# Performance work log

Measured on AMD Instinct MI355X. Metric: run time of the kernel, lower is better.

## Reference

```python
import jax, jax.numpy as jnp
import numpy as np

N, E, IN_DIM, HID, HEADS, LAYERS, NTYPES, NGRAPH = 50000, 600000, 64, 128, 8, 3, 10, 500
C = HID // HEADS
NEG_SLOPE = 0.2
EPS = 1e-5


def setup_inputs() -> dict:
    key = jax.random.key(0)
    ks = jax.random.split(key, 24)
    inp = {
        "x": jax.random.normal(ks[0], (N, IN_DIM), jnp.float32),
        "edge_index": jax.random.randint(ks[1], (2, E), 0, N),
        "node_types": jax.random.randint(ks[2], (N,), 0, NTYPES),
        "batch": jnp.sort(jax.random.randint(ks[3], (N,), 0, NGRAPH)),
        # node embedding linear
        "emb_W": jax.random.normal(ks[4], (IN_DIM, HID), jnp.float32) / np.sqrt(IN_DIM),
        "emb_b": jnp.zeros((HID,), jnp.float32),
        "ntype_emb": jax.random.normal(ks[5], (NTYPES, HID), jnp.float32) * 0.02,
        # stacked GAT layer params
        "gat_W": jax.random.normal(ks[6], (LAYERS, HID, HID), jnp.float32) / np.sqrt(HID),
        "att_src": jax.random.normal(ks[7], (LAYERS, HEADS, C), jnp.float32) * 0.1,
        "att_dst": jax.random.normal(ks[8], (LAYERS, HEADS, C), jnp.float32) * 0.1,
        "gat_b": jnp.zeros((LAYERS, HID), jnp.float32),
        "ln_g": jnp.ones((LAYERS, HID), jnp.float32),
        "ln_b": jnp.zeros((LAYERS, HID), jnp.float32),
        # global attention MLP
        "ga_W1": jax.random.normal(ks[9], (HID, HID), jnp.float32) / np.sqrt(HID),
        "ga_b1": jnp.zeros((HID,), jnp.float32),
        "ga_W2": jax.random.normal(ks[10], (HID, 1), jnp.float32) / np.sqrt(HID),
        "ga_b2": jnp.zeros((1,), jnp.float32),
        # graph classifier head
        "cls_W1": jax.random.normal(ks[11], (HID, HID), jnp.float32) / np.sqrt(HID),
        "cls_b1": jnp.zeros((HID,), jnp.float32),
        "cls_W2": jax.random.normal(ks[12], (HID, 1), jnp.float32) / np.sqrt(HID),
        "cls_b2": jnp.zeros((1,), jnp.float32),
    }
    return inp


def _layer_norm(h, g, b):
    mu = jnp.mean(h, axis=-1, keepdims=True)
    var = jnp.mean(jnp.square(h - mu), axis=-1, keepdims=True)
    return (h - mu) * jax.lax.rsqrt(var + EPS) * g + b


def _gat_layer(h, src, dst, W, a_src, a_dst, bias):
    # h: [N, HID] -> per-head projection [N, H, C]
    hp = (h @ W).reshape(N, HEADS, C)
    alpha_s = jnp.sum(hp * a_src, axis=-1)  # [N, H]
    alpha_d = jnp.sum(hp * a_dst, axis=-1)  # [N, H]
    e = jax.nn.leaky_relu(alpha_s[src] + alpha_d[dst], NEG_SLOPE)  # [E', H]
    # segment softmax over incoming edges of each destination node
    m = jax.ops.segment_max(e, dst, num_segments=N)
    ex = jnp.exp(e - m[dst])
    s = jax.ops.segment_sum(ex, dst, num_segments=N)
    alpha = ex / s[dst]  # every node has a self-loop, so s > 0
    msg = hp[src] * alpha[:, :, None]  # [E', H, C]
    out = jax.ops.segment_sum(msg, dst, num_segments=N)  # [N, H, C]
    return out.reshape(N, HID) + bias


def reference(x, edge_index, node_types, batch, emb_W, emb_b, ntype_emb,
              gat_W, att_src, att_dst, gat_b, ln_g, ln_b,
              ga_W1, ga_b1, ga_W2, ga_b2, cls_W1, cls_b1, cls_W2, cls_b2):
    # self-loops (PyG GATConv add_self_loops=True)
    loop = jnp.arange(N)
    src = jnp.concatenate([edge_index[0], loop])
    dst = jnp.concatenate([edge_index[1], loop])

    h = x @ emb_W + emb_b
    h = h + ntype_emb[node_types]

    for l in range(LAYERS):
        h_prev = h
        h = _gat_layer(h, src, dst, gat_W[l], att_src[l], att_dst[l], gat_b[l])
        h = _layer_norm(h, ln_g[l], ln_b[l])
        h = jax.nn.relu(h + h_prev)

    # global attention pooling: softmax over all nodes (dim 0, as in source)
    scores = jnp.tanh(h @ ga_W1 + ga_b1) @ ga_W2 + ga_b2  # [N, 1]
    attw = jax.nn.softmax(scores, axis=0)
    h_graph = jnp.sum(h * attw, axis=0)  # [HID]

    # global mean pool per graph
    sums = jax.ops.segment_sum(h, batch, num_segments=NGRAPH)  # [G, HID]
    cnts = jax.ops.segment_sum(jnp.ones((N, 1), h.dtype), batch, num_segments=NGRAPH)
    mean_pool = sums / jnp.maximum(cnts, 1.0)

    hg = h_graph + mean_pool  # broadcast [HID] + [G, HID]

    # graph classifier head (features_batch=None path), squeeze(-1)
    out = jax.nn.relu(hg @ cls_W1 + cls_b1) @ cls_W2 + cls_b2
    return out.squeeze(-1)  # [G]
```

## Files before the change

kernel.cpp:

```cpp
#include <hip/hip_runtime.h>
#include <hip/hip_bf16.h>
#include <math.h>

#define HID 128
#define HEADS 8
#define INDIM 64

typedef _Float16 f16x8 __attribute__((ext_vector_type(8)));
typedef _Float16 f16x4 __attribute__((ext_vector_type(4)));
typedef _Float16 f16x2 __attribute__((ext_vector_type(2)));
typedef float f32x4 __attribute__((ext_vector_type(4)));

__device__ __forceinline__ float fast_tanh(float x) {
    return 1.f - 2.f / (__expf(2.f * x) + 1.f);
}

#if defined(__has_builtin)
#if __has_builtin(__builtin_amdgcn_fdot2)
#define HAVE_FDOT2 1
#endif
#endif


__global__ void count_kernel(const int* __restrict__ ei, int* __restrict__ deg, int E, int EE) {
    int e = blockIdx.x * blockDim.x + threadIdx.x;
    if (e >= EE) return;
    int dst = (e < E) ? ei[E + e] : (e - E);
    atomicAdd(&deg[dst], 1);
}

__global__ void block_sum_kernel(const int* __restrict__ deg, int* __restrict__ partials, int N) {
    __shared__ int sdata[4];
    int t = threadIdx.x;
    int i = blockIdx.x * 256 + t;
    int v = (i < N) ? deg[i] : 0;
#pragma unroll
    for (int m = 32; m >= 1; m >>= 1) v += __shfl_xor(v, m, 64);
    if ((t & 63) == 0) sdata[t >> 6] = v;
    __syncthreads();
    if (t == 0) partials[blockIdx.x] = sdata[0] + sdata[1] + sdata[2] + sdata[3];
}

__global__ void scan_partials_kernel(int* __restrict__ partials, int nb) {
    int lane = threadIdx.x;
    int carry = 0;
    for (int base = 0; base < nb; base += 64) {
        int i = base + lane;
        int v = (i < nb) ? partials[i] : 0;
        int orig = v;
#pragma unroll
        for (int off = 1; off < 64; off <<= 1) {
            int x = __shfl_up(v, off, 64);
            if (lane >= off) v += x;
        }
        if (i < nb) partials[i] = v - orig + carry;
        carry += __shfl(v, 63, 64);
    }
}

__global__ void rowptr_kernel(const int* __restrict__ deg, const int* __restrict__ partials,
                              int* __restrict__ rowptr, int* __restrict__ woff, int N, int EE) {
    __shared__ int tmp[256];
    int t = threadIdx.x;
    int i = blockIdx.x * 256 + t;
    int v = (i < N) ? deg[i] : 0;
    tmp[t] = v;
    __syncthreads();
#pragma unroll
    for (int off = 1; off < 256; off <<= 1) {
        int x = (t >= off) ? tmp[t - off] : 0;
        __syncthreads();
        tmp[t] += x;
        __syncthreads();
    }
    int excl = tmp[t] - v + partials[blockIdx.x];
    if (i < N) { rowptr[i] = excl; woff[i] = excl; }
    if (blockIdx.x == 0 && t == 0) rowptr[N] = EE;
}

__global__ void scatter_kernel(const int* __restrict__ ei, int* __restrict__ woff,
                               int* __restrict__ esrc, int E, int EE) {
    int e = blockIdx.x * blockDim.x + threadIdx.x;
    if (e >= EE) return;
    int src, dst;
    if (e < E) { src = ei[e]; dst = ei[E + e]; } else { src = dst = e - E; }
    int slot = atomicAdd(&woff[dst], 1);
    esrc[slot] = src;
}

__global__ void gstart_kernel(const int* __restrict__ batch, int* __restrict__ gstart,
                              int N, int G) {
    int g = blockIdx.x * blockDim.x + threadIdx.x;
    if (g > G) return;
    int lo = 0, hi = N;
    while (lo < hi) {
        int mid = (lo + hi) >> 1;
        if (batch[mid] < g) lo = mid + 1; else hi = mid;
    }
    gstart[g] = lo;
}

__global__ void convert_x_kernel(const float* __restrict__ x, _Float16* __restrict__ x16, int tot4) {
    int i = blockIdx.x * blockDim.x + threadIdx.x;
    if (i >= tot4) return;
    float4 v = ((const float4*)x)[i];
    f16x4 o; o[0] = (_Float16)v.x; o[1] = (_Float16)v.y; o[2] = (_Float16)v.z; o[3] = (_Float16)v.w;
    *(f16x4*)&x16[4 * i] = o;
}

__global__ void convert_w_kernel(const float* __restrict__ emb_W, const float* __restrict__ gat_W,
                                 const float* __restrict__ ga_W1, _Float16* __restrict__ wt_emb,
                                 _Float16* __restrict__ wt_gat, _Float16* __restrict__ wt_ga1) {
    int i = blockIdx.x * blockDim.x + threadIdx.x;
    if (i < 8192) {
        int k = i >> 7, n = i & 127;
        wt_emb[n * 64 + k] = (_Float16)emb_W[i];
    } else if (i < 8192 + 49152) {
        int j = i - 8192;
        int l = j >> 14, r = j & 16383;
        int k = r >> 7, n = r & 127;
        wt_gat[l * 16384 + n * 128 + k] = (_Float16)gat_W[j];
    } else if (i < 73728) {
        int j = i - 57344;
        int k = j >> 7, n = j & 127;
        wt_ga1[n * 128 + k] = (_Float16)ga_W1[j];
    }
}

__global__ __launch_bounds__(256) void mfma_proj_kernel(
    int mode, int K, int N,
    const _Float16* __restrict__ A16, const _Float16* __restrict__ Wt,
    const float* __restrict__ bias, const float* __restrict__ nemb,
    const int* __restrict__ ntypes, _Float16* __restrict__ h16out,
    const float* __restrict__ asrc, const float* __restrict__ adst,
    _Float16* __restrict__ hp_out, float* __restrict__ als, float* __restrict__ ald,
    const float* __restrict__ w2, const float* __restrict__ b2,
    float* __restrict__ escore)
{
    __shared__ _Float16 w_lds[128 * 136];
    __shared__ _Float16 a_lds[64 * 136];
    int t = threadIdx.x;
    int n0 = blockIdx.x * 64;
    int KP = K + 8;

    int K8 = K >> 3;
    for (int i = t; i < 128 * K8; i += 256) {
        int row = i / K8, c8 = i - row * K8;
        *(f16x8*)&w_lds[row * KP + 8 * c8] = *(const f16x8*)&Wt[(size_t)row * K + 8 * c8];
    }
    for (int i = t; i < 64 * K8; i += 256) {
        int row = i / K8, c8 = i - row * K8;
        f16x8 v = {};
        if (n0 + row < N) v = *(const f16x8*)&A16[(size_t)(n0 + row) * K + 8 * c8];
        *(f16x8*)&a_lds[row * KP + 8 * c8] = v;
    }
    __syncthreads();

    int lane = t & 63, wv = t >> 6;
    int l15 = lane & 15, quad = lane >> 4;

    f32x4 acc[8];
#pragma unroll
    for (int c = 0; c < 8; ++c) acc[c] = (f32x4){0.f, 0.f, 0.f, 0.f};

    int ksteps = K >> 5;
    for (int kk = 0; kk < ksteps; ++kk) {
        f16x8 af = *(const f16x8*)&a_lds[(wv * 16 + l15) * KP + kk * 32 + quad * 8];
#pragma unroll
        for (int c = 0; c < 8; ++c) {
            f16x8 bf = *(const f16x8*)&w_lds[(c * 16 + l15) * KP + kk * 32 + quad * 8];
            acc[c] = __builtin_amdgcn_mfma_f32_16x16x32_f16(af, bf, acc[c], 0, 0, 0);
        }
    }

    if (mode == 0) {
        float bv[8];
#pragma unroll
        for (int c = 0; c < 8; ++c) bv[c] = bias[c * 16 + l15];
        __syncthreads();
#pragma unroll
        for (int r = 0; r < 4; ++r) {
            int n = n0 + wv * 16 + quad * 4 + r;
            int nt = (n < N) ? ntypes[n] : 0;
#pragma unroll
            for (int c = 0; c < 8; ++c)
                a_lds[(wv * 16 + quad * 4 + r) * 136 + c * 16 + l15] =
                    (_Float16)(acc[c][r] + bv[c] + nemb[nt * HID + c * 16 + l15]);
        }
        __syncthreads();
        for (int i = t; i < 64 * 16; i += 256) {
            int row = i >> 4, c8 = i & 15;
            int n = n0 + row;
            if (n < N) *(f16x8*)&h16out[(size_t)n * HID + 8 * c8] = *(const f16x8*)&a_lds[row * 136 + 8 * c8];
        }
    } else if (mode == 1) {
        __syncthreads();
#pragma unroll
        for (int c = 0; c < 8; ++c)
#pragma unroll
            for (int r = 0; r < 4; ++r)
                a_lds[(wv * 16 + quad * 4 + r) * 136 + c * 16 + l15] = (_Float16)acc[c][r];
        __syncthreads();
        for (int i = t; i < 64 * 16; i += 256) {
            int row = i >> 4, c8 = i & 15;
            int n = n0 + row;
            if (n < N) *(f16x8*)&hp_out[(size_t)n * HID + 8 * c8] = *(const f16x8*)&a_lds[row * 136 + 8 * c8];
        }
        for (int task = t; task < 512; task += 256) {
            int row = task >> 3, hd = task & 7;
            int n = n0 + row;
            if (n >= N) continue;
            f16x8 v0 = *(const f16x8*)&a_lds[row * 136 + hd * 16];
            f16x8 v1 = *(const f16x8*)&a_lds[row * 136 + hd * 16 + 8];
            float va = 0.f, vd = 0.f;
#pragma unroll
            for (int j = 0; j < 8; ++j) {
                va += (float)v0[j] * asrc[hd * 16 + j] + (float)v1[j] * asrc[hd * 16 + 8 + j];
                vd += (float)v0[j] * adst[hd * 16 + j] + (float)v1[j] * adst[hd * 16 + 8 + j];
            }
            als[n * HEADS + hd] = va;
            ald[n * HEADS + hd] = vd;
        }
    } else {
        float b2v = b2[0];
        float treg[4] = {0.f, 0.f, 0.f, 0.f};
#pragma unroll
        for (int c = 0; c < 8; ++c) {
            float b1v = bias[c * 16 + l15];
            float w2v = w2[c * 16 + l15];
#pragma unroll
            for (int r = 0; r < 4; ++r)
                treg[r] += fast_tanh(acc[c][r] + b1v) * w2v;
        }
#pragma unroll
        for (int r = 0; r < 4; ++r) {
            float v = treg[r];
#pragma unroll
            for (int m = 8; m >= 1; m >>= 1) v += __shfl_xor(v, m, 64);
            if (l15 == 0) {
                int n = n0 + wv * 16 + quad * 4 + r;
                if (n < N) escore[n] = __expf(v + b2v);
            }
        }
    }
}

__global__ void gat_aggregate_kernel(const int* __restrict__ rowptr, const int* __restrict__ esrc,
                                     const float* __restrict__ als, const float* __restrict__ ald,
                                     const _Float16* __restrict__ hp16, const float* __restrict__ gb,
                                     const float* __restrict__ lg, const float* __restrict__ lb,
                                     _Float16* __restrict__ h16, int N) {
    int wave = threadIdx.x >> 6;
    int lane = threadIdx.x & 63;
    int n = blockIdx.x * 4 + wave;
    if (n >= N) return;
    int esub = lane >> 4;
    int cg = lane & 15;
    int hd = cg >> 1;
    float adv = ald[n * HEADS + hd];
    int row = rowptr[n], end = rowptr[n + 1];
    int last = end - 1;
    float acc[8] = {0.f, 0.f, 0.f, 0.f, 0.f, 0.f, 0.f, 0.f};
    float sw = 0.f;
    for (int base = row; base < end; base += 16) {
        int iA = base + esub;
        int iB = iA + 4, iC = iA + 8, iD = iA + 12;
        int cA = iA <= last ? iA : last;
        int cB = iB <= last ? iB : last;
        int cC = iC <= last ? iC : last;
        int cD = iD <= last ? iD : last;
        int sA = esrc[cA], sB = esrc[cB], sC = esrc[cC], sD = esrc[cD];
        f16x8 pA = *(const f16x8*)&hp16[(size_t)sA * HID + cg * 8];
        f16x8 pB = *(const f16x8*)&hp16[(size_t)sB * HID + cg * 8];
        f16x8 pC = *(const f16x8*)&hp16[(size_t)sC * HID + cg * 8];
        f16x8 pD = *(const f16x8*)&hp16[(size_t)sD * HID + cg * 8];
        float aA = als[sA * HEADS + hd];
        float aB = als[sB * HEADS + hd];
        float aC = als[sC * HEADS + hd];
        float aD = als[sD * HEADS + hd];
        float lA = aA + adv; lA = lA > 0.f ? lA : 0.2f * lA;
        float lB = aB + adv; lB = lB > 0.f ? lB : 0.2f * lB;
        float lC = aC + adv; lC = lC > 0.f ? lC : 0.2f * lC;
        float lD = aD + adv; lD = lD > 0.f ? lD : 0.2f * lD;
        float wA = __expf(lA) * ((iA < end) ? 1.f : 0.f);
        float wB = __expf(lB) * ((iB < end) ? 1.f : 0.f);
        float wC = __expf(lC) * ((iC < end) ? 1.f : 0.f);
        float wD = __expf(lD) * ((iD < end) ? 1.f : 0.f);
        sw += (wA + wB) + (wC + wD);
#ifdef HAVE_FDOT2
        f16x2 wAB; wAB[0] = (_Float16)wA; wAB[1] = (_Float16)wB;
        f16x2 wCD; wCD[0] = (_Float16)wC; wCD[1] = (_Float16)wD;
#pragma unroll
        for (int j = 0; j < 8; ++j) {
            f16x2 prAB; prAB[0] = pA[j]; prAB[1] = pB[j];
            f16x2 prCD; prCD[0] = pC[j]; prCD[1] = pD[j];
            acc[j] = __builtin_amdgcn_fdot2(prAB, wAB, acc[j], false);
            acc[j] = __builtin_amdgcn_fdot2(prCD, wCD, acc[j], false);
        }
#else
#pragma unroll
        for (int j = 0; j < 8; ++j)
            acc[j] += wA * (float)pA[j] + wB * (float)pB[j]
                    + wC * (float)pC[j] + wD * (float)pD[j];
#endif
    }
#pragma unroll
    for (int m = 16; m <= 32; m <<= 1) {
        sw += __shfl_xor(sw, m, 64);
#pragma unroll
        for (int j = 0; j < 8; ++j) acc[j] += __shfl_xor(acc[j], m, 64);
    }
    float inv_sw = 1.f / sw;
    float4 g0 = ((const float4*)(gb + cg * 8))[0];
    float4 g1 = ((const float4*)(gb + cg * 8))[1];
    float v[8];
    v[0] = acc[0] * inv_sw + g0.x; v[1] = acc[1] * inv_sw + g0.y;
    v[2] = acc[2] * inv_sw + g0.z; v[3] = acc[3] * inv_sw + g0.w;
    v[4] = acc[4] * inv_sw + g1.x; v[5] = acc[5] * inv_sw + g1.y;
    v[6] = acc[6] * inv_sw + g1.z; v[7] = acc[7] * inv_sw + g1.w;
    float s = 0.f;
#pragma unroll
    for (int j = 0; j < 8; ++j) s += v[j];
#pragma unroll
    for (int m = 32; m >= 1; m >>= 1) s += __shfl_xor(s, m, 64);
    float mu = s * (1.f / 512.f);
    float d[8], sq = 0.f;
#pragma unroll
    for (int j = 0; j < 8; ++j) { d[j] = v[j] - mu; sq += d[j] * d[j]; }
#pragma unroll
    for (int m = 32; m >= 1; m >>= 1) sq += __shfl_xor(sq, m, 64);
    float inv = rsqrtf(sq * (1.f / 512.f) + 1e-5f);
    float4 lg0 = ((const float4*)(lg + cg * 8))[0];
    float4 lg1 = ((const float4*)(lg + cg * 8))[1];
    float4 lb0 = ((const float4*)(lb + cg * 8))[0];
    float4 lb1 = ((const float4*)(lb + cg * 8))[1];
    float lgv[8] = {lg0.x, lg0.y, lg0.z, lg0.w, lg1.x, lg1.y, lg1.z, lg1.w};
    float lbv[8] = {lb0.x, lb0.y, lb0.z, lb0.w, lb1.x, lb1.y, lb1.z, lb1.w};
    f16x8 hold = *(const f16x8*)&h16[(size_t)n * HID + cg * 8];
    f16x8 hnew;
#pragma unroll
    for (int j = 0; j < 8; ++j) {
        float r = d[j] * inv * lgv[j] + lbv[j] + (float)hold[j];
        hnew[j] = (_Float16)(r > 0.f ? r : 0.f);
    }
    if (esub == 0) *(f16x8*)&h16[(size_t)n * HID + cg * 8] = hnew;
}

__global__ void pool_graph_kernel(const _Float16* __restrict__ h16, const float* __restrict__ escore,
                                  const int* __restrict__ gstart, float* __restrict__ sums,
                                  float* __restrict__ cnts, float* __restrict__ hgZ, int G) {
    int g = blockIdx.x;
    int t = threadIdx.x;
    int c = t & 127, grp = t >> 7;
    int s = gstart[g], e = gstart[g + 1];
    float msum = 0.f, asum = 0.f, z = 0.f;
    for (int n = s + grp; n < e; n += 4) {
        float hv = (float)h16[(size_t)n * HID + c];
        float es = escore[n];
        msum += hv;
        asum += es * hv;
        if (c == 0) z += es;
    }
    __shared__ float sm[4][HID];
    __shared__ float sa[4][HID];
    __shared__ float sz[4];
    sm[grp][c] = msum;
    sa[grp][c] = asum;
    if (c == 0) sz[grp] = z;
    __syncthreads();
    if (t < HID) {
        float m = sm[0][t] + sm[1][t] + sm[2][t] + sm[3][t];
        float a = sa[0][t] + sa[1][t] + sa[2][t] + sa[3][t];
        sums[(size_t)g * HID + t] = m;
        atomicAdd(&hgZ[t], a);
    } else if (t == HID) {
        cnts[g] = (float)(e - s);
        atomicAdd(&hgZ[HID], sz[0] + sz[1] + sz[2] + sz[3]);
    }
}

__global__ void head_kernel(const float* __restrict__ hgZ, const float* __restrict__ sums,
                            const float* __restrict__ cnts, const float* __restrict__ W1,
                            const float* __restrict__ b1, const float* __restrict__ W2,
                            const float* __restrict__ b2, float* __restrict__ out, int G) {
    int g = blockIdx.x;
    int t = threadIdx.x;
    __shared__ float hr[HID];
    __shared__ float part[2];
    float Z = hgZ[HID];
    float cnt = cnts[g];
    cnt = cnt > 1.f ? cnt : 1.f;
    hr[t] = hgZ[t] / Z + sums[(size_t)g * HID + t] / cnt;
    __syncthreads();
    float acc = b1[t];
#pragma unroll 8
    for (int k = 0; k < HID; ++k) acc += hr[k] * W1[k * HID + t];
    acc = acc > 0.f ? acc : 0.f;
    float v = acc * W2[t];
#pragma unroll
    for (int m = 32; m >= 1; m >>= 1) v += __shfl_xor(v, m, 64);
    if ((t & 63) == 0) part[t >> 6] = v;
    __syncthreads();
    if (t == 0) out[g] = part[0] + part[1] + b2[0];
}

extern "C" void kernel_launch(void* const* d_in, const int* in_sizes, int n_in,
                              void* d_out, int out_size, void* d_ws, size_t ws_size,
                              hipStream_t stream) {
    const float* x        = (const float*)d_in[0];
    const int*   ei       = (const int*)d_in[1];
    const int*   ntypes   = (const int*)d_in[2];
    const int*   batch    = (const int*)d_in[3];
    const float* emb_W    = (const float*)d_in[4];
    const float* emb_b    = (const float*)d_in[5];
    const float* nemb     = (const float*)d_in[6];
    const float* gat_W    = (const float*)d_in[7];
    const float* att_src  = (const float*)d_in[8];
    const float* att_dst  = (const float*)d_in[9];
    const float* gat_b    = (const float*)d_in[10];
    const float* ln_g     = (const float*)d_in[11];
    const float* ln_b     = (const float*)d_in[12];
    const float* ga_W1    = (const float*)d_in[13];
    const float* ga_b1    = (const float*)d_in[14];
    const float* ga_W2    = (const float*)d_in[15];
    const float* ga_b2    = (const float*)d_in[16];
    const float* cls_W1   = (const float*)d_in[17];
    const float* cls_b1   = (const float*)d_in[18];
    const float* cls_W2   = (const float*)d_in[19];
    const float* cls_b2   = (const float*)d_in[20];
    float* out = (float*)d_out;

    const int N  = in_sizes[2];
    const int E  = in_sizes[1] / 2;
    const int EE = E + N;
    const int G  = out_size;
    const int NB = (N + 255) / 256;

    float* ws      = (float*)d_ws;
    float* als     = ws;
    float* ald     = als + (size_t)N * HEADS;
    float* escore  = ald + (size_t)N * HEADS;
    float* sums    = escore + N;
    float* cnts    = sums + (size_t)G * HID;
    float* hgZ     = cnts + G;
    _Float16* h16  = (_Float16*)(hgZ + HID + 1);
    _Float16* hp16 = h16 + (size_t)N * HID;
    _Float16* x16  = hp16 + (size_t)N * HID;
    _Float16* wt_emb = x16 + (size_t)N * INDIM;
    _Float16* wt_gat = wt_emb + 128 * 64;
    _Float16* wt_ga1 = wt_gat + 3 * 128 * 128;
    int*   rowptr  = (int*)(wt_ga1 + 128 * 128);
    int*   woff    = rowptr + (N + 1);
    int*   deg     = woff + N;
    int*   esrc    = deg + N;
    int*   partials= esrc + EE;
    int*   gstart  = partials + NB;

    hipMemsetAsync(deg, 0, (size_t)N * sizeof(int), stream);
    hipMemsetAsync(hgZ, 0, (HID + 1) * sizeof(float), stream);
    count_kernel<<<(EE + 255) / 256, 256, 0, stream>>>(ei, deg, E, EE);
    block_sum_kernel<<<NB, 256, 0, stream>>>(deg, partials, N);
    scan_partials_kernel<<<1, 64, 0, stream>>>(partials, NB);
    rowptr_kernel<<<NB, 256, 0, stream>>>(deg, partials, rowptr, woff, N, EE);
    scatter_kernel<<<(EE + 255) / 256, 256, 0, stream>>>(ei, woff, esrc, E, EE);
    gstart_kernel<<<(G + 64) / 64, 64, 0, stream>>>(batch, gstart, N, G);
    convert_x_kernel<<<(N * INDIM / 4 + 255) / 256, 256, 0, stream>>>(x, x16, N * INDIM / 4);
    convert_w_kernel<<<(73728 + 255) / 256, 256, 0, stream>>>(
        emb_W, gat_W, ga_W1, wt_emb, wt_gat, wt_ga1);

    const int PB = (N + 63) / 64;

    mfma_proj_kernel<<<PB, 256, 0, stream>>>(
        0, INDIM, N, x16, wt_emb, emb_b, nemb, ntypes, h16,
        nullptr, nullptr, nullptr, nullptr, nullptr, nullptr, nullptr, nullptr);

    for (int l = 0; l < 3; ++l) {
        mfma_proj_kernel<<<PB, 256, 0, stream>>>(
            1, HID, N, h16, wt_gat + (size_t)l * HID * HID,
            nullptr, nullptr, nullptr, nullptr,
            att_src + l * HID, att_dst + l * HID,
            hp16, als, ald, nullptr, nullptr, nullptr);
        gat_aggregate_kernel<<<(N + 3) / 4, 256, 0, stream>>>(
            rowptr, esrc, als, ald, hp16,
            gat_b + l * HID, ln_g + l * HID, ln_b + l * HID, h16, N);
    }

    mfma_proj_kernel<<<PB, 256, 0, stream>>>(
        2, HID, N, h16, wt_ga1, ga_b1, nullptr, nullptr, nullptr,
        nullptr, nullptr, nullptr, nullptr, nullptr, ga_W2, ga_b2, escore);

    pool_graph_kernel<<<G, 512, 0, stream>>>(h16, escore, gstart, sums, cnts, hgZ, G);
    head_kernel<<<G, 128, 0, stream>>>(hgZ, sums, cnts, cls_W1, cls_b1, cls_W2, cls_b2, out, G);
}
```

Measured before the change: 427.6 us.

## Fuse prologue kernels into one launch and process two row tiles per projection block

Merges the degree-count, x conversion, weight transposition, hgZ zeroing and graph-start binary search into a single prologue kernel, removing four launches and a memset. The MFMA projection kernel now loops over two 64-row tiles per block, so the weight tile is loaded into LDS once per 128 rows. The prologue relies on hardcoded index ranges (the gstart offset at 100000 and the hgZ range) that must not overlap other work, and halving the block count lowers parallelism in the projection kernels.

```diff
diff --git a/kernel.cpp b/kernel.cpp
--- a/kernel.cpp
+++ b/kernel.cpp
@@ -21,97 +21,24 @@
 #endif
 #endif
 
-
-__global__ void count_kernel(const int* __restrict__ ei, int* __restrict__ deg, int E, int EE) {
-    int e = blockIdx.x * blockDim.x + threadIdx.x;
-    if (e >= EE) return;
-    int dst = (e < E) ? ei[E + e] : (e - E);
-    atomicAdd(&deg[dst], 1);
-}
-
-__global__ void block_sum_kernel(const int* __restrict__ deg, int* __restrict__ partials, int N) {
-    __shared__ int sdata[4];
-    int t = threadIdx.x;
-    int i = blockIdx.x * 256 + t;
-    int v = (i < N) ? deg[i] : 0;
-#pragma unroll
-    for (int m = 32; m >= 1; m >>= 1) v += __shfl_xor(v, m, 64);
-    if ((t & 63) == 0) sdata[t >> 6] = v;
-    __syncthreads();
-    if (t == 0) partials[blockIdx.x] = sdata[0] + sdata[1] + sdata[2] + sdata[3];
-}
-
-__global__ void scan_partials_kernel(int* __restrict__ partials, int nb) {
-    int lane = threadIdx.x;
-    int carry = 0;
-    for (int base = 0; base < nb; base += 64) {
-        int i = base + lane;
-        int v = (i < nb) ? partials[i] : 0;
-        int orig = v;
-#pragma unroll
-        for (int off = 1; off < 64; off <<= 1) {
-            int x = __shfl_up(v, off, 64);
-            if (lane >= off) v += x;
-        }
-        if (i < nb) partials[i] = v - orig + carry;
-        carry += __shfl(v, 63, 64);
-    }
-}
-
-__global__ void rowptr_kernel(const int* __restrict__ deg, const int* __restrict__ partials,
-                              int* __restrict__ rowptr, int* __restrict__ woff, int N, int EE) {
-    __shared__ int tmp[256];
-    int t = threadIdx.x;
-    int i = blockIdx.x * 256 + t;
-    int v = (i < N) ? deg[i] : 0;
-    tmp[t] = v;
-    __syncthreads();
-#pragma unroll
-    for (int off = 1; off < 256; off <<= 1) {
-        int x = (t >= off) ? tmp[t - off] : 0;
-        __syncthreads();
-        tmp[t] += x;
-        __syncthreads();
-    }
-    int excl = tmp[t] - v + partials[blockIdx.x];
-    if (i < N) { rowptr[i] = excl; woff[i] = excl; }
-    if (blockIdx.x == 0 && t == 0) rowptr[N] = EE;
-}
-
-__global__ void scatter_kernel(const int* __restrict__ ei, int* __restrict__ woff,
-                               int* __restrict__ esrc, int E, int EE) {
-    int e = blockIdx.x * blockDim.x + threadIdx.x;
-    if (e >= EE) return;
-    int src, dst;
-    if (e < E) { src = ei[e]; dst = ei[E + e]; } else { src = dst = e - E; }
-    int slot = atomicAdd(&woff[dst], 1);
-    esrc[slot] = src;
-}
-
-__global__ void gstart_kernel(const int* __restrict__ batch, int* __restrict__ gstart,
-                              int N, int G) {
-    int g = blockIdx.x * blockDim.x + threadIdx.x;
-    if (g > G) return;
-    int lo = 0, hi = N;
-    while (lo < hi) {
-        int mid = (lo + hi) >> 1;
-        if (batch[mid] < g) lo = mid + 1; else hi = mid;
-    }
-    gstart[g] = lo;
-}
-
-__global__ void convert_x_kernel(const float* __restrict__ x, _Float16* __restrict__ x16, int tot4) {
+__global__ void prologue_kernel(const int* __restrict__ ei, int* __restrict__ deg,
+                                const float* __restrict__ x, _Float16* __restrict__ x16,
+                                const float* __restrict__ emb_W, const float* __restrict__ gat_W,
+                                const float* __restrict__ ga_W1, _Float16* __restrict__ wt_emb,
+                                _Float16* __restrict__ wt_gat, _Float16* __restrict__ wt_ga1,
+                                const int* __restrict__ batch, int* __restrict__ gstart,
+                                float* __restrict__ hgZ,
+                                int E, int EE, int N, int G, int XT4) {
     int i = blockIdx.x * blockDim.x + threadIdx.x;
-    if (i >= tot4) return;
-    float4 v = ((const float4*)x)[i];
-    f16x4 o; o[0] = (_Float16)v.x; o[1] = (_Float16)v.y; o[2] = (_Float16)v.z; o[3] = (_Float16)v.w;
-    *(f16x4*)&x16[4 * i] = o;
-}
-
-__global__ void convert_w_kernel(const float* __restrict__ emb_W, const float* __restrict__ gat_W,
-                                 const float* __restrict__ ga_W1, _Float16* __restrict__ wt_emb,
-                                 _Float16* __restrict__ wt_gat, _Float16* __restrict__ wt_ga1) {
-    int i = blockIdx.x * blockDim.x + threadIdx.x;
+    if (i < XT4) {
+        float4 v = ((const float4*)x)[i];
+        f16x4 o; o[0] = (_Float16)v.x; o[1] = (_Float16)v.y; o[2] = (_Float16)v.z; o[3] = (_Float16)v.w;
+        *(f16x4*)&x16[4 * i] = o;
+    }
+    if (i < EE) {
+        int dst = (i < E) ? ei[E + i] : (i - E);
+        atomicAdd(&deg[dst], 1);
+    }
     if (i < 8192) {
         int k = i >> 7, n = i & 127;
         wt_emb[n * 64 + k] = (_Float16)emb_W[i];
@@ -124,7 +51,77 @@
         int j = i - 57344;
         int k = j >> 7, n = j & 127;
         wt_ga1[n * 128 + k] = (_Float16)ga_W1[j];
-    }
+    } else if (i < 73728 + 129) {
+        hgZ[i - 73728] = 0.f;
+    }
+    if (i >= 100000 && i - 100000 <= G) {
+        int g = i - 100000;
+        int lo = 0, hi = N;
+        while (lo < hi) {
+            int mid = (lo + hi) >> 1;
+            if (batch[mid] < g) lo = mid + 1; else hi = mid;
+        }
+        gstart[g] = lo;
+    }
+}
+
+__global__ void block_sum_kernel(const int* __restrict__ deg, int* __restrict__ partials, int N) {
+    __shared__ int sdata[4];
+    int t = threadIdx.x;
+    int i = blockIdx.x * 256 + t;
+    int v = (i < N) ? deg[i] : 0;
+#pragma unroll
+    for (int m = 32; m >= 1; m >>= 1) v += __shfl_xor(v, m, 64);
+    if ((t & 63) == 0) sdata[t >> 6] = v;
+    __syncthreads();
+    if (t == 0) partials[blockIdx.x] = sdata[0] + sdata[1] + sdata[2] + sdata[3];
+}
+
+__global__ void scan_partials_kernel(int* __restrict__ partials, int nb) {
+    int lane = threadIdx.x;
+    int carry = 0;
+    for (int base = 0; base < nb; base += 64) {
+        int i = base + lane;
+        int v = (i < nb) ? partials[i] : 0;
+        int orig = v;
+#pragma unroll
+        for (int off = 1; off < 64; off <<= 1) {
+            int x = __shfl_up(v, off, 64);
+            if (lane >= off) v += x;
+        }
+        if (i < nb) partials[i] = v - orig + carry;
+        carry += __shfl(v, 63, 64);
+    }
+}
+
+__global__ void rowptr_kernel(const int* __restrict__ deg, const int* __restrict__ partials,
+                              int* __restrict__ rowptr, int* __restrict__ woff, int N, int EE) {
+    __shared__ int tmp[256];
+    int t = threadIdx.x;
+    int i = blockIdx.x * 256 + t;
+    int v = (i < N) ? deg[i] : 0;
+    tmp[t] = v;
+    __syncthreads();
+#pragma unroll
+    for (int off = 1; off < 256; off <<= 1) {
+        int x = (t >= off) ? tmp[t - off] : 0;
+        __syncthreads();
+        tmp[t] += x;
+        __syncthreads();
+    }
+    int excl = tmp[t] - v + partials[blockIdx.x];
+    if (i < N) { rowptr[i] = excl; woff[i] = excl; }
+    if (blockIdx.x == 0 && t == 0) rowptr[N] = EE;
+}
+
+__global__ void scatter_kernel(const int* __restrict__ ei, int* __restrict__ woff,
+                               int* __restrict__ esrc, int E, int EE) {
+    int e = blockIdx.x * blockDim.x + threadIdx.x;
+    if (e >= EE) return;
+    int src, dst;
+    if (e < E) { src = ei[e]; dst = ei[E + e]; } else { src = dst = e - E; }
+    int slot = atomicAdd(&woff[dst], 1);
+    esrc[slot] = src;
 }
 
 __global__ __launch_bounds__(256) void mfma_proj_kernel(
@@ -140,106 +137,111 @@
     __shared__ _Float16 w_lds[128 * 136];
     __shared__ _Float16 a_lds[64 * 136];
     int t = threadIdx.x;
-    int n0 = blockIdx.x * 64;
     int KP = K + 8;
-
     int K8 = K >> 3;
+
     for (int i = t; i < 128 * K8; i += 256) {
         int row = i / K8, c8 = i - row * K8;
         *(f16x8*)&w_lds[row * KP + 8 * c8] = *(const f16x8*)&Wt[(size_t)row * K + 8 * c8];
     }
-    for (int i = t; i < 64 * K8; i += 256) {
-        int row = i / K8, c8 = i - row * K8;
-        f16x8 v = {};
-        if (n0 + row < N) v = *(const f16x8*)&A16[(size_t)(n0 + row) * K + 8 * c8];
-        *(f16x8*)&a_lds[row * KP + 8 * c8] = v;
-    }
-    __syncthreads();
 
     int lane = t & 63, wv = t >> 6;
     int l15 = lane & 15, quad = lane >> 4;
 
-    f32x4 acc[8];
-#pragma unroll
-    for (int c = 0; c < 8; ++c) acc[c] = (f32x4){0.f, 0.f, 0.f, 0.f};
-
-    int ksteps = K >> 5;
-    for (int kk = 0; kk < ksteps; ++kk) {
-        f16x8 af = *(const f16x8*)&a_lds[(wv * 16 + l15) * KP + kk * 32 + quad * 8];
-#pragma unroll
-        for (int c = 0; c < 8; ++c) {
-            f16x8 bf = *(const f16x8*)&w_lds[(c * 16 + l15) * KP + kk * 32 + quad * 8];
-            acc[c] = __builtin_amdgcn_mfma_f32_16x16x32_f16(af, bf, acc[c], 0, 0, 0);
-        }
-    }
-
-    if (mode == 0) {
-        float bv[8];
-#pragma unroll
-        for (int c = 0; c < 8; ++c) bv[c] = bias[c * 16 + l15];
+    for (int tile = 0; tile < 2; ++tile) {
+        int n0 = blockIdx.x * 128 + tile * 64;
+        if (n0 >= N) break;
         __syncthreads();
-#pragma unroll
-        for (int r = 0; r < 4; ++r) {
-            int n = n0 + wv * 16 + quad * 4 + r;
-            int nt = (n < N) ? ntypes[n] : 0;
+        for (int i = t; i < 64 * K8; i += 256) {
+            int row = i / K8, c8 = i - row * K8;
+            f16x8 v = {};
+            if (n0 + row < N) v = *(const f16x8*)&A16[(size_t)(n0 + row) * K + 8 * c8];
+            *(f16x8*)&a_lds[row * KP + 8 * c8] = v;
+        }
+        __syncthreads();
+
+        f32x4 acc[8];
+#pragma unroll
+        for (int c = 0; c < 8; ++c) acc[c] = (f32x4){0.f, 0.f, 0.f, 0.f};
+
+        int ksteps = K >> 5;
+        for (int kk = 0; kk < ksteps; ++kk) {
+            f16x8 af = *(const f16x8*)&a_lds[(wv * 16 + l15) * KP + kk * 32 + quad * 8];
+#pragma unroll
+            for (int c = 0; c < 8; ++c) {
+                f16x8 bf = *(const f16x8*)&w_lds[(c * 16 + l15) * KP + kk * 32 + quad * 8];
+                acc[c] = __builtin_amdgcn_mfma_f32_16x16x32_f16(af, bf, acc[c], 0, 0, 0);
+            }
+        }
+
+        if (mode == 0) {
+            float bv[8];
+#pragma unroll
+            for (int c = 0; c < 8; ++c) bv[c] = bias[c * 16 + l15];
+            __syncthreads();
+#pragma unroll
+            for (int r = 0; r < 4; ++r) {
+                int n = n0 + wv * 16 + quad * 4 + r;
+                int nt = (n < N) ? ntypes[n] : 0;
+#pragma unroll
+                for (int c = 0; c < 8; ++c)
+                    a_lds[(wv * 16 + quad * 4 + r) * 136 + c * 16 + l15] =
+                        (_Float16)(acc[c][r] + bv[c] + nemb[nt * HID + c * 16 + l15]);
+            }
+            __syncthreads();
+            for (int i = t; i < 64 * 16; i += 256) {
+                int row = i >> 4, c8 = i & 15;
+                int n = n0 + row;
+                if (n < N) *(f16x8*)&h16out[(size_t)n * HID + 8 * c8] = *(const f16x8*)&a_lds[row * 136 + 8 * c8];
+            }
+        } else if (mode == 1) {
+            __syncthreads();
 #pragma unroll
             for (int c = 0; c < 8; ++c)
-                a_lds[(wv * 16 + quad * 4 + r) * 136 + c * 16 + l15] =
-                    (_Float16)(acc[c][r] + bv[c] + nemb[nt * HID + c * 16 + l15]);
-        }
-        __syncthreads();
-        for (int i = t; i < 64 * 16; i += 256) {
-            int row = i >> 4, c8 = i & 15;
-            int n = n0 + row;
-            if (n < N) *(f16x8*)&h16out[(size_t)n * HID + 8 * c8] = *(const f16x8*)&a_lds[row * 136 + 8 * c8];
-        }
-    } else if (mode == 1) {
-        __syncthreads();
-#pragma unroll
-        for (int c = 0; c < 8; ++c)
-#pragma unroll
-            for (int r = 0; r < 4; ++r)
-                a_lds[(wv * 16 + quad * 4 + r) * 136 + c * 16 + l15] = (_Float16)acc[c][r];
-        __syncthreads();
-        for (int i = t; i < 64 * 16; i += 256) {
-            int row = i >> 4, c8 = i & 15;
-            int n = n0 + row;
-            if (n < N) *(f16x8*)&hp_out[(size_t)n * HID + 8 * c8] = *(const f16x8*)&a_lds[row * 136 + 8 * c8];
-        }
-        for (int task = t; task < 512; task += 256) {
-            int row = task >> 3, hd = task & 7;
-            int n = n0 + row;
-            if (n >= N) continue;
-            f16x8 v0 = *(const f16x8*)&a_lds[row * 136 + hd * 16];
-            f16x8 v1 = *(const f16x8*)&a_lds[row * 136 + hd * 16 + 8];
-            float va = 0.f, vd = 0.f;
-#pragma unroll
-            for (int j = 0; j < 8; ++j) {
-                va += (float)v0[j] * asrc[hd * 16 + j] + (float)v1[j] * asrc[hd * 16 + 8 + j];
-                vd += (float)v0[j] * adst[hd * 16 + j] + (float)v1[j] * adst[hd * 16 + 8 + j];
-            }
-            als[n * HEADS + hd] = va;
-            ald[n * HEADS + hd] = vd;
-        }
-    } else {
-        float b2v = b2[0];
-        float treg[4] = {0.f, 0.f, 0.f, 0.f};
-#pragma unroll
-        for (int c = 0; c < 8; ++c) {
-            float b1v = bias[c * 16 + l15];
-            float w2v = w2[c * 16 + l15];
-#pragma unroll
-            for (int r = 0; r < 4; ++r)
-                treg[r] += fast_tanh(acc[c][r] + b1v) * w2v;
-        }
-#pragma unroll
-        for (int r = 0; r < 4; ++r) {
-            float v = treg[r];
-#pragma unroll
-            for (int m = 8; m >= 1; m >>= 1) v += __shfl_xor(v, m, 64);
-            if (l15 == 0) {
-                int n = n0 + wv * 16 + quad * 4 + r;
-                if (n < N) escore[n] = __expf(v + b2v);
+#pragma unroll
+                for (int r = 0; r < 4; ++r)
+                    a_lds[(wv * 16 + quad * 4 + r) * 136 + c * 16 + l15] = (_Float16)acc[c][r];
+            __syncthreads();
+            for (int i = t; i < 64 * 16; i += 256) {
+                int row = i >> 4, c8 = i & 15;
+                int n = n0 + row;
+                if (n < N) *(f16x8*)&hp_out[(size_t)n * HID + 8 * c8] = *(const f16x8*)&a_lds[row * 136 + 8 * c8];
+            }
+            for (int task = t; task < 512; task += 256) {
+                int row = task >> 3, hd = task & 7;
+                int n = n0 + row;
+                if (n >= N) continue;
+                f16x8 v0 = *(const f16x8*)&a_lds[row * 136 + hd * 16];
+                f16x8 v1 = *(const f16x8*)&a_lds[row * 136 + hd * 16 + 8];
+                float va = 0.f, vd = 0.f;
+#pragma unroll
+                for (int j = 0; j < 8; ++j) {
+                    va += (float)v0[j] * asrc[hd * 16 + j] + (float)v1[j] * asrc[hd * 16 + 8 + j];
+                    vd += (float)v0[j] * adst[hd * 16 + j] + (float)v1[j] * adst[hd * 16 + 8 + j];
+                }
+                als[n * HEADS + hd] = va;
+                ald[n * HEADS + hd] = vd;
+            }
+        } else {
+            float b2v = b2[0];
+            float treg[4] = {0.f, 0.f, 0.f, 0.f};
+#pragma unroll
+            for (int c = 0; c < 8; ++c) {
+                float b1v = bias[c * 16 + l15];
+                float w2v = w2[c * 16 + l15];
+#pragma unroll
+                for (int r = 0; r < 4; ++r)
+                    treg[r] += fast_tanh(acc[c][r] + b1v) * w2v;
+            }
+#pragma unroll
+            for (int r = 0; r < 4; ++r) {
+                float v = treg[r];
+#pragma unroll
+                for (int m = 8; m >= 1; m >>= 1) v += __shfl_xor(v, m, 64);
+                if (l15 == 0) {
+                    int n = n0 + wv * 16 + quad * 4 + r;
+                    if (n < N) escore[n] = __expf(v + b2v);
+                }
             }
         }
     }
@@ -435,6 +437,7 @@
     const int EE = E + N;
     const int G  = out_size;
     const int NB = (N + 255) / 256;
+    const int XT4 = N * INDIM / 4;
 
     float* ws      = (float*)d_ws;
     float* als     = ws;
@@ -457,18 +460,17 @@
     int*   gstart  = partials + NB;
 
     hipMemsetAsync(deg, 0, (size_t)N * sizeof(int), stream);
-    hipMemsetAsync(hgZ, 0, (HID + 1) * sizeof(float), stream);
-    count_kernel<<<(EE + 255) / 256, 256, 0, stream>>>(ei, deg, E, EE);
+    int ptot = XT4 > EE ? XT4 : EE;
+    if (ptot < 100000 + G + 1) ptot = 100000 + G + 1;
+    prologue_kernel<<<(ptot + 255) / 256, 256, 0, stream>>>(
+        ei, deg, x, x16, emb_W, gat_W, ga_W1, wt_emb, wt_gat, wt_ga1,
+        batch, gstart, hgZ, E, EE, N, G, XT4);
     block_sum_kernel<<<NB, 256, 0, stream>>>(deg, partials, N);
     scan_partials_kernel<<<1, 64, 0, stream>>>(partials, NB);
     rowptr_kernel<<<NB, 256, 0, stream>>>(deg, partials, rowptr, woff, N, EE);
     scatter_kernel<<<(EE + 255) / 256, 256, 0, stream>>>(ei, woff, esrc, E, EE);
-    gstart_kernel<<<(G + 64) / 64, 64, 0, stream>>>(batch, gstart, N, G);
-    convert_x_kernel<<<(N * INDIM / 4 + 255) / 256, 256, 0, stream>>>(x, x16, N * INDIM / 4);
-    convert_w_kernel<<<(73728 + 255) / 256, 256, 0, stream>>>(
-        emb_W, gat_W, ga_W1, wt_emb, wt_gat, wt_ga1);
-
-    const int PB = (N + 63) / 64;
+
+    const int PB = (N + 127) / 128;
 
     mfma_proj_kernel<<<PB, 256, 0, stream>>>(
         0, INDIM, N, x16, wt_emb, emb_b, nemb, ntypes, h16,
```

Result: faster. 402.3 us (-5.9%).
